# Optimization experiments

Measured on AMD Instinct MI355X. Metric: run time of the kernel, lower is better.

Reference implementation:

```python
import jax, jax.numpy as jnp
import numpy as np

N = 2000
E = 128
H = 8
DH = E // H
K = 32  # max_neighbors
CLAMP = 1e4


def _sanitize(t):
    t = jnp.nan_to_num(t, nan=0.0, posinf=CLAMP, neginf=-CLAMP)
    return jnp.clip(t, -CLAMP, CLAMP)


def _layernorm(h, g, b, eps=1e-5):
    mu = h.mean(-1, keepdims=True)
    var = ((h - mu) ** 2).mean(-1, keepdims=True)
    return (h - mu) * jax.lax.rsqrt(var + eps) * g + b


def setup_inputs() -> dict:
    key = jax.random.key(0)
    ks = jax.random.split(key, 8)
    x = jax.random.normal(ks[0], (N, E), dtype=jnp.float32)
    coords9 = jax.random.normal(ks[1], (N, 9), dtype=jnp.float32)
    prompt_signal = jax.random.normal(ks[2], (E,), dtype=jnp.float32)
    pe_w = jax.random.normal(ks[3], (3, 32), dtype=jnp.float32) / np.sqrt(3.0)
    pe_b = jnp.zeros((32,), jnp.float32)
    pe_g = jnp.ones((32,), jnp.float32)
    pe_bt = jnp.zeros((32,), jnp.float32)
    in_w = jax.random.normal(ks[4], (3 * E, E), dtype=jnp.float32) / np.sqrt(E)
    in_b = jnp.zeros((3 * E,), jnp.float32)
    out_w = jax.random.normal(ks[5], (E, E), dtype=jnp.float32) / np.sqrt(E)
    out_b = jnp.zeros((E,), jnp.float32)
    return {"x": x, "coords9": coords9, "prompt_signal": prompt_signal,
            "pe_w": pe_w, "pe_b": pe_b, "pe_g": pe_g, "pe_bt": pe_bt,
            "in_w": in_w, "in_b": in_b, "out_w": out_w, "out_b": out_b}


def reference(x, coords9, prompt_signal, pe_w, pe_b, pe_g, pe_bt, in_w, in_b, out_w, out_b):
    n = x.shape[0]
    verts = coords9.reshape(n, 3, 3)
    cent = verts.mean(axis=1)  # (N,3)

    # pairwise centroid distances (only geo-relation channel that affects the output;
    # cos_angles/area_ratios/boundary_sharing feed geo_bias which is dead code in forward)
    diff = cent[:, None, :] - cent[None, :, :]
    dist = jnp.sqrt(jnp.sum(diff * diff, axis=-1) + 1e-20)  # (N,N)

    # positional encoder: Linear(3,32) -> GELU(exact) -> LayerNorm(32)
    pe = jax.nn.gelu(cent @ pe_w + pe_b, approximate=False)
    pe = _layernorm(pe, pe_g, pe_bt)  # (N,32)

    prompt_enhanced = x + prompt_signal[None, :]
    pos_enhanced = jnp.concatenate([prompt_enhanced[:, : 3 * E // 4], pe], axis=-1)  # (N,128)

    # top-K nearest neighbors -> additive attention mask (0 for kept, -inf-like otherwise)
    _, topk_idx = jax.lax.top_k(-dist, K)  # (N,K) smallest distances
    big_neg = jnp.float32(-1e9)
    attn_mask = jnp.full((n, n), big_neg, dtype=jnp.float32)
    attn_mask = attn_mask.at[jnp.arange(n)[:, None], topk_idx].set(0.0)

    # nn.MultiheadAttention (self-attention, eval mode -> no dropout)
    qkv = pos_enhanced @ in_w.T + in_b  # (N,3E)
    q, k, v = jnp.split(qkv, 3, axis=-1)
    q = q.reshape(n, H, DH).transpose(1, 0, 2)  # (H,N,DH)
    k = k.reshape(n, H, DH).transpose(1, 0, 2)
    v = v.reshape(n, H, DH).transpose(1, 0, 2)
    scores = jnp.einsum('hnd,hmd->hnm', q, k) / np.sqrt(DH) + attn_mask[None]
    probs = jax.nn.softmax(scores, axis=-1)
    o = jnp.einsum('hnm,hmd->hnd', probs, v)  # (H,N,DH)
    o = o.transpose(1, 0, 2).reshape(n, E)
    out = o @ out_w.T + out_b
    return _sanitize(out)
```

## Files before the change

kernel.cpp:

```cpp
#include <hip/hip_runtime.h>
#include <math.h>

#define N_NODES 2000
#define E_DIM   128
#define QKV_W   384
#define LDA     36

__global__ __launch_bounds__(256) void prep_qkv_kernel(
    const float* __restrict__ x, const float* __restrict__ coords9,
    const float* __restrict__ ps, const float* __restrict__ pe_w,
    const float* __restrict__ pe_b, const float* __restrict__ pe_g,
    const float* __restrict__ pe_bt, const float* __restrict__ in_w,
    const float* __restrict__ in_b,
    float* __restrict__ cx_, float* __restrict__ cy_, float* __restrict__ cz_,
    float* __restrict__ qkv)
{
    __shared__ __align__(16) float As[E_DIM * LDA];
    int tid = threadIdx.x;
    int rt = blockIdx.x / 3, ct = blockIdx.x % 3;
    int rbase = rt * 32, cbase = ct * 128;
    int g = tid >> 5, lane = tid & 31;

    #pragma unroll
    for (int rr = 0; rr < 4; ++rr) {
        int rl = rr * 8 + g;
        int row = rbase + rl;
        bool vr = (row < N_NODES);
        float cx = 0.f, cy = 0.f, cz = 0.f;
        if (vr) {
            const float* c9 = coords9 + row * 9;
            cx = (c9[0] + c9[3] + c9[6]) * (1.0f / 3.0f);
            cy = (c9[1] + c9[4] + c9[7]) * (1.0f / 3.0f);
            cz = (c9[2] + c9[5] + c9[8]) * (1.0f / 3.0f);
        }
        if (ct == 0 && vr && lane == 0) { cx_[row] = cx; cy_[row] = cy; cz_[row] = cz; }

        #pragma unroll
        for (int k = 0; k < 3; ++k) {
            int c = lane + 32 * k;
            float v = vr ? (x[row * E_DIM + c] + ps[c]) : 0.f;
            As[c * LDA + rl] = v;
        }

        int j = lane;
        float h = cx * pe_w[j] + cy * pe_w[32 + j] + cz * pe_w[64 + j] + pe_b[j];
        float ge = 0.5f * h * (1.0f + erff(h * 0.7071067811865476f));
        float s = ge;
        #pragma unroll
        for (int m = 16; m >= 1; m >>= 1) s += __shfl_xor(s, m);
        float mu = s * (1.0f / 32.0f);
        float d = ge - mu;
        float v2 = d * d;
        #pragma unroll
        for (int m = 16; m >= 1; m >>= 1) v2 += __shfl_xor(v2, m);
        float var = v2 * (1.0f / 32.0f);
        float y = d * (1.0f / sqrtf(var + 1e-5f)) * pe_g[j] + pe_bt[j];
        As[(96 + j) * LDA + rl] = vr ? y : 0.f;
    }
    __syncthreads();

    int cg = tid & 31, rg = tid >> 5;
    int c0 = cbase + cg * 4, r0 = rg * 4;
    float acc[4][4];
    #pragma unroll
    for (int i = 0; i < 4; ++i)
        #pragma unroll
        for (int jj = 0; jj < 4; ++jj) acc[i][jj] = 0.f;

    for (int k0 = 0; k0 < 128; k0 += 4) {
        float4 a0 = *(const float4*)&As[(k0 + 0) * LDA + r0];
        float4 a1 = *(const float4*)&As[(k0 + 1) * LDA + r0];
        float4 a2 = *(const float4*)&As[(k0 + 2) * LDA + r0];
        float4 a3 = *(const float4*)&As[(k0 + 3) * LDA + r0];
        #pragma unroll
        for (int ci = 0; ci < 4; ++ci) {
            float4 b = *(const float4*)&in_w[(c0 + ci) * E_DIM + k0];
            acc[0][ci] += a0.x * b.x + a1.x * b.y + a2.x * b.z + a3.x * b.w;
            acc[1][ci] += a0.y * b.x + a1.y * b.y + a2.y * b.z + a3.y * b.w;
            acc[2][ci] += a0.z * b.x + a1.z * b.y + a2.z * b.z + a3.z * b.w;
            acc[3][ci] += a0.w * b.x + a1.w * b.y + a2.w * b.z + a3.w * b.w;
        }
    }

    #pragma unroll
    for (int ri = 0; ri < 4; ++ri) {
        int row = rbase + r0 + ri;
        if (row < N_NODES) {
            float4 o4;
            o4.x = acc[ri][0] + in_b[c0 + 0];
            o4.y = acc[ri][1] + in_b[c0 + 1];
            o4.z = acc[ri][2] + in_b[c0 + 2];
            o4.w = acc[ri][3] + in_b[c0 + 3];
            *(float4*)&qkv[row * QKV_W + c0] = o4;
        }
    }
}

__device__ __forceinline__ float sanitize(float v)
{
    v = (v == v) ? v : 0.f;
    return fminf(fmaxf(v, -1e4f), 1e4f);
}

__global__ __launch_bounds__(256) void attn_proj_kernel(
    const float* __restrict__ cx_, const float* __restrict__ cy_,
    const float* __restrict__ cz_, const float* __restrict__ qkv,
    const float* __restrict__ out_w, const float* __restrict__ out_b,
    float* __restrict__ out)
{
    __shared__ unsigned int hist[256];
    __shared__ float wMin[4], wMax[4];
    __shared__ float sh_lo, sh_scale;
    __shared__ int sh_b, sh_nless, sh_sel, sh_eq;
    __shared__ int waveSum[4];
    __shared__ int topk[32];
    __shared__ int eqIdx[256];
    __shared__ unsigned int eqKey[256];
    __shared__ __align__(16) float qs[128];
    __shared__ float pr[256];
    __shared__ __align__(16) float os[128];

    int tid = threadIdx.x;
    int row = blockIdx.x;
    int lane = tid & 63, wid = tid >> 6;

    float cix = cx_[row], ciy = cy_[row], ciz = cz_[row];
    unsigned int kbits[8];
    bool valid[8];
    float lmin = __int_as_float(0x7f800000);
    float lmax = __int_as_float(0xff800000);
    {
        #pragma clang fp contract(off)
        #pragma unroll
        for (int l = 0; l < 8; ++l) {
            int j = tid + 256 * l;
            valid[l] = (j < N_NODES);
            float key = __int_as_float(0x7f800000);
            if (valid[l]) {
                float dx = cix - cx_[j];
                float dy = ciy - cy_[j];
                float dz = ciz - cz_[j];
                float a = dx * dx;
                float b = dy * dy;
                float c = dz * dz;
                float d2 = ((a + b) + c) + 1e-20f;
                key = sqrtf(d2);
                lmin = fminf(lmin, key);
                lmax = fmaxf(lmax, key);
            }
            kbits[l] = __float_as_uint(key);
        }
    }

    #pragma unroll
    for (int m = 32; m >= 1; m >>= 1) {
        lmin = fminf(lmin, __shfl_xor(lmin, m));
        lmax = fmaxf(lmax, __shfl_xor(lmax, m));
    }
    if (lane == 0) { wMin[wid] = lmin; wMax[wid] = lmax; }
    hist[tid] = 0u;
    if (tid == 0) { sh_sel = 0; sh_eq = 0; }
    __syncthreads();
    if (tid == 0) {
        float lo = fminf(fminf(wMin[0], wMin[1]), fminf(wMin[2], wMin[3]));
        float hi = fmaxf(fmaxf(wMax[0], wMax[1]), fmaxf(wMax[2], wMax[3]));
        sh_lo = lo;
        sh_scale = 255.0f / fmaxf(hi - lo, 1e-30f);
    }
    __syncthreads();
    float lo = sh_lo, scale = sh_scale;

    #pragma unroll
    for (int l = 0; l < 8; ++l) {
        if (valid[l]) {
            float key = __uint_as_float(kbits[l]);
            int bin = (int)((key - lo) * scale);
            bin = min(max(bin, 0), 255);
            atomicAdd(&hist[bin], 1u);
        }
    }
    __syncthreads();

    int h = (int)hist[tid];
    int incl = h;
    #pragma unroll
    for (int dd = 1; dd < 64; dd <<= 1) {
        int u = __shfl_up(incl, dd);
        if (lane >= dd) incl += u;
    }
    if (lane == 63) waveSum[wid] = incl;
    __syncthreads();
    int off = 0;
    for (int w = 0; w < wid; ++w) off += waveSum[w];
    int cum = incl + off;
    if (cum >= 32 && (cum - h) < 32) {
        sh_b = tid;
        sh_nless = cum - h;
    }
    __syncthreads();

    int b = sh_b;
    int req = 32 - sh_nless;

    #pragma unroll
    for (int l = 0; l < 8; ++l) {
        if (valid[l]) {
            float key = __uint_as_float(kbits[l]);
            int bin = (int)((key - lo) * scale);
            bin = min(max(bin, 0), 255);
            int j = tid + 256 * l;
            if (bin < b) {
                int p = atomicAdd(&sh_sel, 1);
                topk[p] = j;
            } else if (bin == b) {
                int e = atomicAdd(&sh_eq, 1);
                if (e < 256) { eqIdx[e] = j; eqKey[e] = kbits[l]; }
            }
        }
    }
    if (tid < 128) qs[tid] = qkv[row * QKV_W + tid];
    __syncthreads();

    int eq = min(sh_eq, 256);
    if (tid < eq) {
        int myIdx = eqIdx[tid];
        unsigned int myKey = eqKey[tid];
        int rank = 0;
        for (int u = 0; u < eq; ++u) {
            unsigned int ku = eqKey[u];
            rank += (ku < myKey || (ku == myKey && eqIdx[u] < myIdx)) ? 1 : 0;
        }
        if (rank < req) {
            int p = atomicAdd(&sh_sel, 1);
            topk[p] = myIdx;
        }
    }
    __syncthreads();

    {
        int hh = tid >> 5, j = tid & 31;
        int jj = topk[j];
        const float4* kp = (const float4*)&qkv[jj * QKV_W + 128 + hh * 16];
        const float4* qp = (const float4*)&qs[hh * 16];
        float s = 0.f;
        #pragma unroll
        for (int i = 0; i < 4; ++i) {
            float4 kv = kp[i], qv = qp[i];
            s += qv.x * kv.x + qv.y * kv.y + qv.z * kv.z + qv.w * kv.w;
        }
        s *= 0.25f;
        float m = s;
        #pragma unroll
        for (int msk = 16; msk >= 1; msk >>= 1) m = fmaxf(m, __shfl_xor(m, msk));
        float p = expf(s - m);
        float su = p;
        #pragma unroll
        for (int msk = 16; msk >= 1; msk >>= 1) su += __shfl_xor(su, msk);
        pr[tid] = p / su;
    }
    __syncthreads();

    if (tid < 128) {
        int hh = tid >> 4;
        float acc = 0.f;
        #pragma unroll
        for (int j = 0; j < 32; ++j) {
            int jj = topk[j];
            acc += pr[hh * 32 + j] * qkv[jj * QKV_W + 256 + tid];
        }
        os[tid] = acc;
    }
    __syncthreads();

    if (tid < 128) {
        const float* wr = out_w + tid * E_DIM;
        float a = 0.f;
        #pragma unroll
        for (int e = 0; e < 128; e += 4) {
            float4 w4 = *(const float4*)&wr[e];
            float4 o4 = *(const float4*)&os[e];
            a += o4.x * w4.x + o4.y * w4.y + o4.z * w4.z + o4.w * w4.w;
        }
        out[row * E_DIM + tid] = sanitize(a + out_b[tid]);
    }
}

extern "C" void kernel_launch(void* const* d_in, const int* in_sizes, int n_in,
                              void* d_out, int out_size, void* d_ws, size_t ws_size,
                              hipStream_t stream)
{
    const float* x      = (const float*)d_in[0];
    const float* coords = (const float*)d_in[1];
    const float* ps     = (const float*)d_in[2];
    const float* pe_w   = (const float*)d_in[3];
    const float* pe_b   = (const float*)d_in[4];
    const float* pe_g   = (const float*)d_in[5];
    const float* pe_bt  = (const float*)d_in[6];
    const float* in_w   = (const float*)d_in[7];
    const float* in_b   = (const float*)d_in[8];
    const float* out_w  = (const float*)d_in[9];
    const float* out_b  = (const float*)d_in[10];
    float* out = (float*)d_out;

    float* ws  = (float*)d_ws;
    float* cxp = ws;
    float* cyp = ws + 2048;
    float* czp = ws + 4096;
    float* qkvb = ws + 6144;

    prep_qkv_kernel<<<189, 256, 0, stream>>>(x, coords, ps, pe_w, pe_b, pe_g, pe_bt,
                                             in_w, in_b, cxp, cyp, czp, qkvb);
    attn_proj_kernel<<<2000, 256, 0, stream>>>(cxp, cyp, czp, qkvb, out_w, out_b, out);
}
```

Before: 123.8 us.

## Process one query row per wavefront instead of per block

Restructures the attention kernel so each 64-lane wavefront handles one row end to end, with four rows per block and 500 blocks. Block-wide barriers and cross-wave shared reductions become wave-local shuffles and wave barriers, and the histogram scan packs four bins per lane. This targets the many __syncthreads and idle threads in the per-row top-k selection and attention. In exchange each lane now holds 32 distance keys in registers, raising register pressure and possibly lowering occupancy, and the grid has fewer blocks.

```diff
diff --git a/kernel.cpp b/kernel.cpp
--- a/kernel.cpp
+++ b/kernel.cpp
@@ -108,140 +108,139 @@
     const float* __restrict__ out_w, const float* __restrict__ out_b,
     float* __restrict__ out)
 {
-    __shared__ unsigned int hist[256];
-    __shared__ float wMin[4], wMax[4];
-    __shared__ float sh_lo, sh_scale;
-    __shared__ int sh_b, sh_nless, sh_sel, sh_eq;
-    __shared__ int waveSum[4];
-    __shared__ int topk[32];
-    __shared__ int eqIdx[256];
-    __shared__ unsigned int eqKey[256];
-    __shared__ __align__(16) float qs[128];
-    __shared__ float pr[256];
-    __shared__ __align__(16) float os[128];
+    __shared__ __align__(16) unsigned int hist[4][256];
+    __shared__ int eqIdx[4][256];
+    __shared__ unsigned int eqKey[4][256];
+    __shared__ int topk[4][32];
+    __shared__ int cnt[4][2];
+    __shared__ __align__(16) float qs[4][128];
+    __shared__ __align__(16) float pr[4][256];
+    __shared__ __align__(16) float os[4][128];
 
     int tid = threadIdx.x;
-    int row = blockIdx.x;
-    int lane = tid & 63, wid = tid >> 6;
+    int lane = tid & 63, w = tid >> 6;
+    int row = blockIdx.x * 4 + w;
 
     float cix = cx_[row], ciy = cy_[row], ciz = cz_[row];
-    unsigned int kbits[8];
-    bool valid[8];
+
+    unsigned int kb[32];
     float lmin = __int_as_float(0x7f800000);
     float lmax = __int_as_float(0xff800000);
     {
         #pragma clang fp contract(off)
         #pragma unroll
-        for (int l = 0; l < 8; ++l) {
-            int j = tid + 256 * l;
-            valid[l] = (j < N_NODES);
+        for (int it = 0; it < 32; ++it) {
+            int j = lane + 64 * it;
             float key = __int_as_float(0x7f800000);
-            if (valid[l]) {
+            if (j < N_NODES) {
                 float dx = cix - cx_[j];
                 float dy = ciy - cy_[j];
                 float dz = ciz - cz_[j];
                 float a = dx * dx;
-                float b = dy * dy;
+                float b2 = dy * dy;
                 float c = dz * dz;
-                float d2 = ((a + b) + c) + 1e-20f;
+                float d2 = ((a + b2) + c) + 1e-20f;
                 key = sqrtf(d2);
                 lmin = fminf(lmin, key);
                 lmax = fmaxf(lmax, key);
             }
-            kbits[l] = __float_as_uint(key);
-        }
-    }
-
+            kb[it] = __float_as_uint(key);
+        }
+    }
     #pragma unroll
     for (int m = 32; m >= 1; m >>= 1) {
         lmin = fminf(lmin, __shfl_xor(lmin, m));
         lmax = fmaxf(lmax, __shfl_xor(lmax, m));
     }
-    if (lane == 0) { wMin[wid] = lmin; wMax[wid] = lmax; }
-    hist[tid] = 0u;
-    if (tid == 0) { sh_sel = 0; sh_eq = 0; }
-    __syncthreads();
-    if (tid == 0) {
-        float lo = fminf(fminf(wMin[0], wMin[1]), fminf(wMin[2], wMin[3]));
-        float hi = fmaxf(fmaxf(wMax[0], wMax[1]), fmaxf(wMax[2], wMax[3]));
-        sh_lo = lo;
-        sh_scale = 255.0f / fmaxf(hi - lo, 1e-30f);
-    }
-    __syncthreads();
-    float lo = sh_lo, scale = sh_scale;
-
-    #pragma unroll
-    for (int l = 0; l < 8; ++l) {
-        if (valid[l]) {
-            float key = __uint_as_float(kbits[l]);
+    float lo = lmin;
+    float scale = 255.0f / fmaxf(lmax - lmin, 1e-30f);
+
+    *(uint4*)&hist[w][4 * lane] = make_uint4(0u, 0u, 0u, 0u);
+    if (lane == 0) { cnt[w][0] = 0; cnt[w][1] = 0; }
+    __builtin_amdgcn_wave_barrier();
+    #pragma unroll
+    for (int it = 0; it < 32; ++it) {
+        int j = lane + 64 * it;
+        if (j < N_NODES) {
+            float key = __uint_as_float(kb[it]);
             int bin = (int)((key - lo) * scale);
             bin = min(max(bin, 0), 255);
-            atomicAdd(&hist[bin], 1u);
-        }
-    }
-    __syncthreads();
-
-    int h = (int)hist[tid];
-    int incl = h;
+            atomicAdd(&hist[w][bin], 1u);
+        }
+    }
+    __builtin_amdgcn_wave_barrier();
+
+    uint4 h4 = *(const uint4*)&hist[w][4 * lane];
+    int s0 = (int)h4.x;
+    int s1 = s0 + (int)h4.y;
+    int s2 = s1 + (int)h4.z;
+    int tot = s2 + (int)h4.w;
+    int incl = tot;
     #pragma unroll
     for (int dd = 1; dd < 64; dd <<= 1) {
         int u = __shfl_up(incl, dd);
         if (lane >= dd) incl += u;
     }
-    if (lane == 63) waveSum[wid] = incl;
-    __syncthreads();
-    int off = 0;
-    for (int w = 0; w < wid; ++w) off += waveSum[w];
-    int cum = incl + off;
-    if (cum >= 32 && (cum - h) < 32) {
-        sh_b = tid;
-        sh_nless = cum - h;
-    }
-    __syncthreads();
-
-    int b = sh_b;
-    int req = 32 - sh_nless;
-
-    #pragma unroll
-    for (int l = 0; l < 8; ++l) {
-        if (valid[l]) {
-            float key = __uint_as_float(kbits[l]);
+    int excl = incl - tot;
+    int c0 = excl + s0, c1 = excl + s1, c2 = excl + s2, c3 = excl + tot;
+    int cand = 256, candN = 0;
+    if (excl < 32 && c0 >= 32)      { cand = 4 * lane;     candN = excl; }
+    else if (c0 < 32 && c1 >= 32)   { cand = 4 * lane + 1; candN = c0; }
+    else if (c1 < 32 && c2 >= 32)   { cand = 4 * lane + 2; candN = c1; }
+    else if (c2 < 32 && c3 >= 32)   { cand = 4 * lane + 3; candN = c2; }
+    int candV = (cand << 8) | candN;
+    #pragma unroll
+    for (int m = 32; m >= 1; m >>= 1) candV = min(candV, __shfl_xor(candV, m));
+    int b = candV >> 8;
+    int req = 32 - (candV & 255);
+
+    #pragma unroll
+    for (int it = 0; it < 32; ++it) {
+        int j = lane + 64 * it;
+        if (j < N_NODES) {
+            float key = __uint_as_float(kb[it]);
             int bin = (int)((key - lo) * scale);
             bin = min(max(bin, 0), 255);
-            int j = tid + 256 * l;
             if (bin < b) {
-                int p = atomicAdd(&sh_sel, 1);
-                topk[p] = j;
+                int p = atomicAdd(&cnt[w][0], 1);
+                topk[w][p] = j;
             } else if (bin == b) {
-                int e = atomicAdd(&sh_eq, 1);
-                if (e < 256) { eqIdx[e] = j; eqKey[e] = kbits[l]; }
+                int e = atomicAdd(&cnt[w][1], 1);
+                if (e < 256) { eqIdx[w][e] = j; eqKey[w][e] = kb[it]; }
             }
         }
     }
-    if (tid < 128) qs[tid] = qkv[row * QKV_W + tid];
-    __syncthreads();
-
-    int eq = min(sh_eq, 256);
-    if (tid < eq) {
-        int myIdx = eqIdx[tid];
-        unsigned int myKey = eqKey[tid];
+    qs[w][lane]      = qkv[row * QKV_W + lane];
+    qs[w][lane + 64] = qkv[row * QKV_W + lane + 64];
+    __builtin_amdgcn_wave_barrier();
+
+    int eq = min(cnt[w][1], 256);
+    for (int e = lane; e < eq; e += 64) {
+        int myIdx = eqIdx[w][e];
+        unsigned int myKey = eqKey[w][e];
         int rank = 0;
         for (int u = 0; u < eq; ++u) {
-            unsigned int ku = eqKey[u];
-            rank += (ku < myKey || (ku == myKey && eqIdx[u] < myIdx)) ? 1 : 0;
+            unsigned int ku = eqKey[w][u];
+            rank += (ku < myKey || (ku == myKey && eqIdx[w][u] < myIdx)) ? 1 : 0;
         }
         if (rank < req) {
-            int p = atomicAdd(&sh_sel, 1);
-            topk[p] = myIdx;
-        }
-    }
-    __syncthreads();
-
-    {
-        int hh = tid >> 5, j = tid & 31;
-        int jj = topk[j];
+            int p = atomicAdd(&cnt[w][0], 1);
+            topk[w][p] = myIdx;
+        }
+    }
+    __builtin_amdgcn_wave_barrier();
+
+    int tk[32];
+    #pragma unroll
+    for (int sl = 0; sl < 32; ++sl) tk[sl] = topk[w][sl];
+
+    #pragma unroll
+    for (int pp = 0; pp < 4; ++pp) {
+        int p = lane + 64 * pp;
+        int hh = p >> 5, sl = p & 31;
+        int jj = tk[sl];
         const float4* kp = (const float4*)&qkv[jj * QKV_W + 128 + hh * 16];
-        const float4* qp = (const float4*)&qs[hh * 16];
+        const float4* qp = (const float4*)&qs[w][hh * 16];
         float s = 0.f;
         #pragma unroll
         for (int i = 0; i < 4; ++i) {
@@ -252,36 +251,39 @@
         float m = s;
         #pragma unroll
         for (int msk = 16; msk >= 1; msk >>= 1) m = fmaxf(m, __shfl_xor(m, msk));
-        float p = expf(s - m);
-        float su = p;
+        float pe = expf(s - m);
+        float su = pe;
         #pragma unroll
         for (int msk = 16; msk >= 1; msk >>= 1) su += __shfl_xor(su, msk);
-        pr[tid] = p / su;
-    }
-    __syncthreads();
-
-    if (tid < 128) {
-        int hh = tid >> 4;
+        pr[w][p] = pe / su;
+    }
+    __builtin_amdgcn_wave_barrier();
+
+    #pragma unroll
+    for (int cc = 0; cc < 2; ++cc) {
+        int c = lane + 64 * cc;
+        int hh = c >> 4;
         float acc = 0.f;
         #pragma unroll
-        for (int j = 0; j < 32; ++j) {
-            int jj = topk[j];
-            acc += pr[hh * 32 + j] * qkv[jj * QKV_W + 256 + tid];
-        }
-        os[tid] = acc;
-    }
-    __syncthreads();
-
-    if (tid < 128) {
-        const float* wr = out_w + tid * E_DIM;
+        for (int sl = 0; sl < 32; ++sl) {
+            acc += pr[w][hh * 32 + sl] * qkv[tk[sl] * QKV_W + 256 + c];
+        }
+        os[w][c] = acc;
+    }
+    __builtin_amdgcn_wave_barrier();
+
+    #pragma unroll
+    for (int cc = 0; cc < 2; ++cc) {
+        int c = lane + 64 * cc;
+        const float* wr = out_w + c * E_DIM;
         float a = 0.f;
         #pragma unroll
         for (int e = 0; e < 128; e += 4) {
             float4 w4 = *(const float4*)&wr[e];
-            float4 o4 = *(const float4*)&os[e];
+            float4 o4 = *(const float4*)&os[w][e];
             a += o4.x * w4.x + o4.y * w4.y + o4.z * w4.z + o4.w * w4.w;
         }
-        out[row * E_DIM + tid] = sanitize(a + out_b[tid]);
+        out[row * E_DIM + c] = sanitize(a + out_b[c]);
     }
 }
 
@@ -310,5 +312,5 @@
 
     prep_qkv_kernel<<<189, 256, 0, stream>>>(x, coords, ps, pe_w, pe_b, pe_g, pe_bt,
                                              in_w, in_b, cxp, cyp, czp, qkvb);
-    attn_proj_kernel<<<2000, 256, 0, stream>>>(cxp, cyp, czp, qkvb, out_w, out_b, out);
+    attn_proj_kernel<<<500, 256, 0, stream>>>(cxp, cyp, czp, qkvb, out_w, out_b, out);
 }
```

Measured after the change: 137.9 us. 1.11x slower.
